# Kernel tuning notes

Measured on AMD Instinct MI355X. Metric: run time of the kernel, lower is better.

Reference implementation:

```python
import jax, jax.numpy as jnp
import numpy as np

B, NP, NM, C, H = 4, 256, 128, 128, 128
EPS = 1e-5

def layernorm(x, g, b):
    mu = jnp.mean(x, axis=-1, keepdims=True)
    var = jnp.var(x, axis=-1, keepdims=True)
    return (x - mu) * jax.lax.rsqrt(var + EPS) * g + b

def setup_inputs() -> dict:
    key = jax.random.key(0)
    ks = jax.random.split(key, 16)
    s = lambda d: 1.0 / np.sqrt(d)
    return {
        "z": jax.random.normal(ks[0], (B, NP, NM, C), jnp.float32),
        "z_mask": jnp.ones((B, NP, NM), jnp.float32),
        "pocket_pair": jax.random.normal(ks[1], (B, NP, NP, C), jnp.float32),
        "mol_pair": jax.random.normal(ks[2], (B, NM, NM, C), jnp.float32),
        "ln_g": jnp.ones((C,), jnp.float32), "ln_b": jnp.zeros((C,), jnp.float32),
        "lnh_g": jnp.ones((H,), jnp.float32), "lnh_b": jnp.zeros((H,), jnp.float32),
        "gw1": jax.random.uniform(ks[3], (C, H), jnp.float32, -s(C), s(C)),
        "gb1": jnp.zeros((H,), jnp.float32),
        "gw2": jax.random.uniform(ks[4], (C, H), jnp.float32, -s(C), s(C)),
        "gb2": jnp.zeros((H,), jnp.float32),
        "w1": jax.random.uniform(ks[5], (C, H), jnp.float32, -s(C), s(C)),
        "b1": jnp.zeros((H,), jnp.float32),
        "w2": jax.random.uniform(ks[6], (C, H), jnp.float32, -s(C), s(C)),
        "b2": jnp.zeros((H,), jnp.float32),
        "egw": jax.random.uniform(ks[7], (C, C), jnp.float32, -s(C), s(C)),
        "egb": jnp.zeros((C,), jnp.float32),
        "asw": jax.random.uniform(ks[8], (H, C), jnp.float32, -s(H), s(H)),
        "asb": jnp.zeros((C,), jnp.float32),
    }

def reference(z, z_mask, pocket_pair, mol_pair, ln_g, ln_b, lnh_g, lnh_b,
              gw1, gb1, gw2, gb2, w1, b1, w2, b2, egw, egb, asw, asb):
    m = z_mask[..., None]                      # [b,Np,Nm,1]
    zn = layernorm(z, ln_g, ln_b)              # [b,Np,Nm,C]
    pp = layernorm(pocket_pair, ln_g, ln_b)    # [b,Np,Np,C]
    mp = layernorm(mol_pair, ln_g, ln_b)       # [b,Nm,Nm,C]
    gate1 = lambda x: jax.nn.sigmoid(x @ gw1 + gb1) * (x @ w1 + b1)
    gate2 = lambda x: jax.nn.sigmoid(x @ gw2 + gb2) * (x @ w2 + b2)
    ab1 = gate1(zn) * m                        # [b,Np,Nm,H]
    ab2 = gate2(zn) * m                        # [b,Np,Nm,H]
    ppg = gate2(pp)                            # [b,Np,Np,H]
    mpg = gate1(mp)                            # [b,Nm,Nm,H]
    block1 = jnp.einsum('bikc,bkjc->bijc', ppg, ab1)   # [b,Np,Nm,H]
    block2 = jnp.einsum('bikc,bjkc->bijc', ab2, mpg)   # [b,Np,Nm,H]
    h = layernorm(block1 + block2, lnh_g, lnh_b)
    out = jax.nn.sigmoid(zn @ egw + egb) * (h @ asw + asb) * m
    return out
```

## Files before the change

kernel.cpp:

```cpp
#include <hip/hip_runtime.h>
#include <hip/hip_bf16.h>

#define DEVFN __device__ __forceinline__
using bf16 = __hip_bfloat16;
typedef __attribute__((ext_vector_type(8))) short short8;
typedef __attribute__((ext_vector_type(4))) float f32x4;
typedef __attribute__((ext_vector_type(4))) unsigned short us4;

constexpr int BB = 4, NP = 256, NM = 128, CC = 128, HH = 128;
constexpr float EPS = 1e-5f;

#define MFMA16(a,b,c) __builtin_amdgcn_mfma_f32_16x16x32_bf16((a),(b),(c),0,0,0)

DEVFN unsigned short bfbits(float v){ union{ bf16 b; unsigned short s; } u; u.b = __float2bfloat16(v); return u.s; }
DEVFN float bits2f(unsigned short s){ union{ unsigned int i; float f; } u; u.i = ((unsigned)s) << 16; return u.f; }
DEVFN float sigm(float x){ return 1.0f / (1.0f + __expf(-x)); }


__global__ __launch_bounds__(256)
void prep_weights_kernel(const float* __restrict__ gw1, const float* __restrict__ w1,
                         const float* __restrict__ gw2, const float* __restrict__ w2,
                         const float* __restrict__ egw, const float* __restrict__ asw,
                         bf16* __restrict__ wt)
{
  __shared__ float wl[128][129];
  const int bx = blockIdx.x;
  const float* W = (bx==0)?gw1 : (bx==1)?w1 : (bx==2)?gw2 : (bx==3)?w2 : (bx==4)?egw : asw;
  const int t = threadIdx.x;
  for (int i = 0; i < 16; ++i){
    int idx = t + 256*i;
    int k = idx >> 5, n0 = (idx & 31) * 4;
    float4 v = *reinterpret_cast<const float4*>(W + k*128 + n0);
    wl[k][n0] = v.x; wl[k][n0+1] = v.y; wl[k][n0+2] = v.z; wl[k][n0+3] = v.w;
  }
  __syncthreads();
  short* o = reinterpret_cast<short*>(wt) + bx * 16384;
  const int n = t >> 1, kh = t & 1;
  #pragma unroll
  for (int j = 0; j < 8; ++j){
    short8 p;
    #pragma unroll
    for (int u = 0; u < 8; ++u) p[u] = (short)bfbits(wl[kh*64 + j*8 + u][n]);
    *reinterpret_cast<short8*>(o + n*128 + kh*64 + j*8) = p;
  }
}

struct GateSmem {
  short xs[128*128];
  float lgb[2][128];
  float mk[128];
};

DEVFN void gate_pass(const char* xb, const float* mk, int t, long obase,
                     const short* wtg, const short* wtl,
                     const float* __restrict__ bgp, const float* __restrict__ blp,
                     bf16* outp)
{
  const int l = t & 63, w = t >> 6, lr = l & 15, lg = l >> 4;
  const int n0 = w * 32;
  short8 bgf[2][4], blf[2][4];
  #pragma unroll
  for (int nt = 0; nt < 2; ++nt)
    #pragma unroll
    for (int ks = 0; ks < 4; ++ks){
      int n = n0 + nt*16 + lr, ko = ks*32 + lg*8;
      bgf[nt][ks] = *reinterpret_cast<const short8*>(wtg + n*128 + ko);
      blf[nt][ks] = *reinterpret_cast<const short8*>(wtl + n*128 + ko);
    }
  float bgv[2] = { bgp[n0 + lr], bgp[n0 + 16 + lr] };
  float blv[2] = { blp[n0 + lr], blp[n0 + 16 + lr] };
  unsigned short* ob = reinterpret_cast<unsigned short*>(outp);

  for (int mt = 0; mt < 8; ++mt){
    f32x4 zv = {0.f,0.f,0.f,0.f};
    f32x4 ag0 = zv, ag1 = zv, al0 = zv, al1 = zv;
    #pragma unroll
    for (int ks = 0; ks < 4; ++ks){
      int m = mt*16 + lr, ko = ks*32 + lg*8;
      short8 a = *reinterpret_cast<const short8*>(xb + ((m*256 + ko*2) ^ ((m & 7) << 4)));
      ag0 = MFMA16(a, bgf[0][ks], ag0);
      al0 = MFMA16(a, blf[0][ks], al0);
      ag1 = MFMA16(a, bgf[1][ks], ag1);
      al1 = MFMA16(a, blf[1][ks], al1);
    }
    #pragma unroll
    for (int nt = 0; nt < 2; ++nt){
      f32x4 ag = nt ? ag1 : ag0, al = nt ? al1 : al0;
      int h = n0 + nt*16 + lr;
      us4 pk;
      #pragma unroll
      for (int rg = 0; rg < 4; ++rg){
        int rowl = mt*16 + lg*4 + rg;
        float val = sigm(ag[rg] + bgv[nt]) * (al[rg] + blv[nt]) * mk[rowl];
        pk[rg] = bfbits(val);
      }
      *reinterpret_cast<us4*>(ob + obase + h*128 + mt*16 + lg*4) = pk;
    }
  }
}

DEVFN void eg_pass(const char* xb, int t, long obase,
                   const short* wtg, const float* __restrict__ bgp, bf16* outp)
{
  const int l = t & 63, w = t >> 6, lr = l & 15, lg = l >> 4;
  const int n0 = w * 32;
  short8 bgf[2][4];
  #pragma unroll
  for (int nt = 0; nt < 2; ++nt)
    #pragma unroll
    for (int ks = 0; ks < 4; ++ks){
      int n = n0 + nt*16 + lr, ko = ks*32 + lg*8;
      bgf[nt][ks] = *reinterpret_cast<const short8*>(wtg + n*128 + ko);
    }
  float bgv[2] = { bgp[n0 + lr], bgp[n0 + 16 + lr] };
  unsigned short* ob = reinterpret_cast<unsigned short*>(outp);

  for (int mt = 0; mt < 8; ++mt){
    f32x4 zv = {0.f,0.f,0.f,0.f};
    f32x4 ag0 = zv, ag1 = zv;
    #pragma unroll
    for (int ks = 0; ks < 4; ++ks){
      int m = mt*16 + lr, ko = ks*32 + lg*8;
      short8 a = *reinterpret_cast<const short8*>(xb + ((m*256 + ko*2) ^ ((m & 7) << 4)));
      ag0 = MFMA16(a, bgf[0][ks], ag0);
      ag1 = MFMA16(a, bgf[1][ks], ag1);
    }
    #pragma unroll
    for (int nt = 0; nt < 2; ++nt){
      f32x4 ag = nt ? ag1 : ag0;
      int h = n0 + nt*16 + lr;
      us4 pk;
      #pragma unroll
      for (int rg = 0; rg < 4; ++rg) pk[rg] = bfbits(sigm(ag[rg] + bgv[nt]));
      *reinterpret_cast<us4*>(ob + obase + h*128 + mt*16 + lg*4) = pk;
    }
  }
}

constexpr int NZB = (BB*NP*NM)/128;
constexpr int NPB = (BB*NP*NP)/128;
constexpr int NMB = (BB*NM*NM)/128;

__global__ __launch_bounds__(256, 3)
void gate_all_kernel(const float* __restrict__ z, const float* __restrict__ zmask,
                     const float* __restrict__ pp, const float* __restrict__ mp,
                     const float* __restrict__ lng, const float* __restrict__ lnb,
                     const bf16* __restrict__ wt,
                     const float* __restrict__ gb1, const float* __restrict__ b1,
                     const float* __restrict__ gb2, const float* __restrict__ b2,
                     const float* __restrict__ egbv,
                     bf16* ab1, bf16* ab2, bf16* egp, bf16* ppg, bf16* mpg)
{
  __shared__ GateSmem sm;
  const int t = threadIdx.x;
  const short* wts = reinterpret_cast<const short*>(wt);

  int bx = blockIdx.x;
  const float* x; const float* mask = nullptr;
  long R; int npass = 1;
  const short *w1g, *w1l; const float *bg1v, *bl1v; bf16* o1;
  if (bx < NZB){
    x = z; mask = zmask; R = (long)NP*NM; npass = 3;
    w1g = wts + 0*16384; w1l = wts + 1*16384; bg1v = gb1; bl1v = b1; o1 = ab1;
  } else if (bx < NZB + NPB){
    bx -= NZB; x = pp; R = (long)NP*NP;
    w1g = wts + 2*16384; w1l = wts + 3*16384; bg1v = gb2; bl1v = b2; o1 = ppg;
  } else {
    bx -= NZB + NPB; x = mp; R = (long)NM*NM;
    w1g = wts + 0*16384; w1l = wts + 1*16384; bg1v = gb1; bl1v = b1; o1 = mpg;
  }
  const long row0 = (long)bx * 128;
  const int b = (int)(row0 / R);
  const long rowb = row0 - (long)b * R;
  const long obase = ((long)b * (R >> 7) + (rowb >> 7)) * 16384;

  if (t < 128){
    sm.lgb[0][t] = lng[t];
    sm.lgb[1][t] = lnb[t];
    sm.mk[t] = mask ? mask[row0 + t] : 1.0f;
  }

  const int r = t >> 1, hf = t & 1;
  const float4* xrow = reinterpret_cast<const float4*>(x + (row0 + r)*128 + hf*64);
  float4 vb[16];
  float s = 0.f, ss = 0.f;
  #pragma unroll
  for (int i = 0; i < 16; ++i){
    float4 v = xrow[i]; vb[i] = v;
    s  += v.x + v.y + v.z + v.w;
    ss += v.x*v.x + v.y*v.y + v.z*v.z + v.w*v.w;
  }
  s  += __shfl_xor(s, 1);
  ss += __shfl_xor(ss, 1);
  const float mu = s * (1.f/128.f);
  const float rsg = rsqrtf(ss * (1.f/128.f) - mu*mu + EPS);
  __syncthreads();
  {
    char* xbw = reinterpret_cast<char*>(sm.xs);
    #pragma unroll
    for (int j = 0; j < 8; ++j){
      float4 a = vb[2*j], c2 = vb[2*j+1];
      float vv[8] = {a.x, a.y, a.z, a.w, c2.x, c2.y, c2.z, c2.w};
      short8 p;
      #pragma unroll
      for (int u = 0; u < 8; ++u){
        int ch = hf*64 + j*8 + u;
        p[u] = (short)bfbits((vv[u] - mu) * rsg * sm.lgb[0][ch] + sm.lgb[1][ch]);
      }
      *reinterpret_cast<short8*>(xbw + ((r*256 + hf*128 + j*16) ^ ((r & 7) << 4))) = p;
    }
  }
  __syncthreads();

  const char* xb = reinterpret_cast<const char*>(sm.xs);
  gate_pass(xb, sm.mk, t, obase, w1g, w1l, bg1v, bl1v, o1);
  if (npass == 3){
    gate_pass(xb, sm.mk, t, obase, wts + 2*16384, wts + 3*16384, gb2, b2, ab2);
    eg_pass(xb, t, obase, wts + 4*16384, egbv, egp);
  }
}

DEVFN int b1swz(int j){ return (((j & 7) ^ ((j >> 3) & 7)) << 4); }

__global__ __launch_bounds__(256, 2)
void einsum_mfma_kernel(const bf16* __restrict__ ppg, const bf16* __restrict__ ab1,
                        const bf16* __restrict__ ab2, const bf16* __restrict__ mpg,
                        bf16* __restrict__ bsum)
{
  __shared__ short b1t[128*256];
  const int t = threadIdx.x, l = t & 63, w = t >> 6, lr = l & 15, lg = l >> 4;
  const int bc = blockIdx.x;
  const int b = bc >> 7, c = bc & 127;
  const short* A1s = reinterpret_cast<const short*>(ppg);
  const short* B1s = reinterpret_cast<const short*>(ab1);
  const short* A2s = reinterpret_cast<const short*>(ab2);
  const short* B2s = reinterpret_cast<const short*>(mpg);
  const long a1base = ((long)b*512*128 + c) * 128;
  const long b1base = ((long)b*256*128 + c) * 128;
  const long a2base = ((long)b*256*128 + c) * 128;
  const long b2base = ((long)b*128*128 + c) * 128;

  char* lb = reinterpret_cast<char*>(b1t);
  for (int it = 0; it < 16; ++it){
    int idx = t + 256*it;
    int k = idx >> 4, j0 = (idx & 15) * 8;
    short8 v = *reinterpret_cast<const short8*>(B1s + b1base + (long)k*16384 + j0);
    #pragma unroll
    for (int u = 0; u < 8; ++u){
      int j = j0 + u;
      *reinterpret_cast<short*>(lb + ((j*512 + k*2) ^ b1swz(j))) = v[u];
    }
  }
  __syncthreads();

  f32x4 zv = {0.f,0.f,0.f,0.f};
  f32x4 acc[4][8];
  #pragma unroll
  for (int i = 0; i < 4; ++i)
    #pragma unroll
    for (int j = 0; j < 8; ++j) acc[i][j] = zv;

  const int m0 = w * 64;
  for (int ks = 0; ks < 8; ++ks){
    int ko = ks*32 + lg*8;
    int koh = ko >> 7, kol = ko & 127;
    short8 af[4];
    #pragma unroll
    for (int mt = 0; mt < 4; ++mt){
      long m = m0 + mt*16 + lr;
      af[mt] = *reinterpret_cast<const short8*>(A1s + a1base + m*32768 + (long)koh*16384 + kol);
    }
    short8 bf[8];
    #pragma unroll
    for (int nt = 0; nt < 8; ++nt){
      int n = nt*16 + lr;
      bf[nt] = *reinterpret_cast<const short8*>(lb + ((n*512 + ko*2) ^ b1swz(n)));
    }
    #pragma unroll
    for (int mt = 0; mt < 4; ++mt)
      #pragma unroll
      for (int nt = 0; nt < 8; ++nt)
        acc[mt][nt] = MFMA16(af[mt], bf[nt], acc[mt][nt]);
  }
  for (int ks = 0; ks < 4; ++ks){
    int ko = ks*32 + lg*8;
    short8 af[4];
    #pragma unroll
    for (int mt = 0; mt < 4; ++mt){
      long m = m0 + mt*16 + lr;
      af[mt] = *reinterpret_cast<const short8*>(A2s + a2base + m*16384 + ko);
    }
    short8 bf[8];
    #pragma unroll
    for (int nt = 0; nt < 8; ++nt){
      long n = nt*16 + lr;
      bf[nt] = *reinterpret_cast<const short8*>(B2s + b2base + n*16384 + ko);
    }
    #pragma unroll
    for (int mt = 0; mt < 4; ++mt)
      #pragma unroll
      for (int nt = 0; nt < 8; ++nt)
        acc[mt][nt] = MFMA16(af[mt], bf[nt], acc[mt][nt]);
  }
  unsigned short* out = reinterpret_cast<unsigned short*>(bsum) + (long)bc * (NP*NM);
  #pragma unroll
  for (int mt = 0; mt < 4; ++mt)
    #pragma unroll
    for (int nt = 0; nt < 8; ++nt)
      #pragma unroll
      for (int rg = 0; rg < 4; ++rg)
        out[(m0 + mt*16 + lg*4 + rg)*128 + nt*16 + lr] = bfbits(acc[mt][nt][rg]);
}

__global__ __launch_bounds__(256, 2)
void final_mfma_kernel(const bf16* __restrict__ bsum, const bf16* __restrict__ eg,
                       const float* __restrict__ mask,
                       const float* __restrict__ lnhg, const float* __restrict__ lnhb,
                       const bf16* __restrict__ wt, const float* __restrict__ asb,
                       float* __restrict__ out)
{
  __shared__ struct {
    short xsT[128][72];
    short xs[64*128];
    float lgb[2][128];
    float ps[4][64], pss[4][64];
    float mu[64], rs[64], mk[64];
  } sm;
  const int t = threadIdx.x, l = t & 63, w = t >> 6, lr = l & 15, lg = l >> 4;
  const long row0 = (long)blockIdx.x * 64;
  const int b = (int)(row0 >> 15);
  const long rowb = row0 & 32767;

  if (t < 128){ sm.lgb[0][t] = lnhg[t]; sm.lgb[1][t] = lnhb[t]; }
  if (t < 64) sm.mk[t] = mask[row0 + t];

  const short* bs = reinterpret_cast<const short*>(bsum);
  #pragma unroll
  for (int i = 0; i < 4; ++i){
    int idx = t + 256*i;
    int c = idx >> 3, j8 = idx & 7;
    short8 v = *reinterpret_cast<const short8*>(bs + (long)(b*128 + c)*32768 + rowb + j8*8);
    *reinterpret_cast<short8*>(&sm.xsT[c][j8*8]) = v;
  }
  __syncthreads();
  {
    int ij = t & 63, q = t >> 6;
    float s = 0.f, ss = 0.f;
    #pragma unroll
    for (int k = 0; k < 32; ++k){
      float v = bits2f((unsigned short)sm.xsT[q*32 + k][ij]);
      s += v; ss += v*v;
    }
    sm.ps[q][ij] = s; sm.pss[q][ij] = ss;
  }
  __syncthreads();
  if (t < 64){
    float s  = sm.ps[0][t] + sm.ps[1][t] + sm.ps[2][t] + sm.ps[3][t];
    float ss = sm.pss[0][t] + sm.pss[1][t] + sm.pss[2][t] + sm.pss[3][t];
    float mu = s * (1.f/128.f);
    float var = ss * (1.f/128.f) - mu*mu;
    sm.mu[t] = mu; sm.rs[t] = rsqrtf(var + EPS);
  }
  __syncthreads();
  {
    int ij = t & 63, q = t >> 6;
    float mu = sm.mu[ij], rg2 = sm.rs[ij];
    char* xbw = reinterpret_cast<char*>(sm.xs);
    #pragma unroll
    for (int u = 0; u < 4; ++u){
      short8 p;
      #pragma unroll
      for (int e = 0; e < 8; ++e){
        int c = q*32 + u*8 + e;
        float v = bits2f((unsigned short)sm.xsT[c][ij]);
        p[e] = (short)bfbits((v - mu) * rg2 * sm.lgb[0][c] + sm.lgb[1][c]);
      }
      *reinterpret_cast<short8*>(xbw + ((ij*256 + q*64 + u*16) ^ ((ij & 7) << 4))) = p;
    }
  }
  __syncthreads();

  const short* aswt = reinterpret_cast<const short*>(wt) + 5*16384;
  f32x4 zv = {0.f,0.f,0.f,0.f};
  f32x4 acc[8];
  #pragma unroll
  for (int i = 0; i < 8; ++i) acc[i] = zv;
  const char* xb = reinterpret_cast<const char*>(sm.xs);
  #pragma unroll
  for (int ks = 0; ks < 4; ++ks){
    int m = w*16 + lr, ko = ks*32 + lg*8;
    short8 a = *reinterpret_cast<const short8*>(xb + ((m*256 + ko*2) ^ ((m & 7) << 4)));
    #pragma unroll
    for (int nt = 0; nt < 8; ++nt){
      short8 bfr = *reinterpret_cast<const short8*>(aswt + (nt*16 + lr)*128 + ko);
      acc[nt] = MFMA16(a, bfr, acc[nt]);
    }
  }
  const unsigned short* egb2 = reinterpret_cast<const unsigned short*>(eg);
  const long egbase = ((long)b*256 + (rowb >> 7)) * 16384;
  const int rsub = (int)(rowb & 64);
  #pragma unroll
  for (int nt = 0; nt < 8; ++nt){
    int co = nt*16 + lr;
    float bias = asb[co];
    us4 egv = *reinterpret_cast<const us4*>(egb2 + egbase + co*128 + rsub + w*16 + lg*4);
    #pragma unroll
    for (int rg = 0; rg < 4; ++rg){
      int rowl = w*16 + lg*4 + rg;
      float val = bits2f(egv[rg]) * (acc[nt][rg] + bias) * sm.mk[rowl];
      out[(row0 + rowl)*128 + co] = val;
    }
  }
}

extern "C" void kernel_launch(void* const* d_in, const int* in_sizes, int n_in,
                              void* d_out, int out_size, void* d_ws, size_t ws_size,
                              hipStream_t stream)
{
  const float* z     = (const float*)d_in[0];
  const float* zmask = (const float*)d_in[1];
  const float* pp    = (const float*)d_in[2];
  const float* mp    = (const float*)d_in[3];
  const float* ln_g  = (const float*)d_in[4];
  const float* ln_b  = (const float*)d_in[5];
  const float* lnh_g = (const float*)d_in[6];
  const float* lnh_b = (const float*)d_in[7];
  const float* gw1   = (const float*)d_in[8];
  const float* gb1   = (const float*)d_in[9];
  const float* gw2   = (const float*)d_in[10];
  const float* gb2   = (const float*)d_in[11];
  const float* w1    = (const float*)d_in[12];
  const float* b1    = (const float*)d_in[13];
  const float* w2    = (const float*)d_in[14];
  const float* b2    = (const float*)d_in[15];
  const float* egw   = (const float*)d_in[16];
  const float* egb   = (const float*)d_in[17];
  const float* asw   = (const float*)d_in[18];
  const float* asb   = (const float*)d_in[19];
  float* out = (float*)d_out;

  const size_t ZE = (size_t)BB*NP*NM*HH;
  const size_t PE = (size_t)BB*NP*NP*HH;
  const size_t ME = (size_t)BB*NM*NM*HH;
  char* ws = (char*)d_ws;
  size_t off = 0;
  bf16* wt   = (bf16*)(ws + off); off += 6 * 16384 * 2;
  bf16* ab1  = (bf16*)(ws + off); off += ZE * 2;
  bf16* ab2  = (bf16*)(ws + off); off += ZE * 2;
  bf16* egp  = (bf16*)(ws + off); off += ZE * 2;
  bf16* ppg  = (bf16*)(ws + off); off += PE * 2;
  bf16* mpg  = (bf16*)(ws + off); off += ME * 2;
  bf16* bsum = (bf16*)(ws + off); off += ZE * 2;
  if (ws_size < off) return;

  prep_weights_kernel<<<6, 256, 0, stream>>>(gw1, w1, gw2, w2, egw, asw, wt);

  gate_all_kernel<<<NZB + NPB + NMB, 256, 0, stream>>>(
      z, zmask, pp, mp, ln_g, ln_b, wt,
      gb1, b1, gb2, b2, egb,
      ab1, ab2, egp, ppg, mpg);

  einsum_mfma_kernel<<<BB*CC, 256, 0, stream>>>(ppg, ab1, ab2, mpg, bsum);

  final_mfma_kernel<<<(BB*NP*NM)/64, 256, 0, stream>>>(
      bsum, egp, zmask, lnh_g, lnh_b, wt, asb, out);
}
```

Measured before the change: 245.7 us.

## Process two row tiles per gate block, prefetching the second during compute

Each gate_all block now handles two consecutive 128-row tiles and the grid is halved. The second tile's fp32 input is loaded into registers before the first tile's gate and eg MFMA passes run, so global load latency overlaps with compute. The cost is that 64 extra floats per thread stay live across the MFMA passes. Under the launch bound of 3 blocks per SM this can raise register pressure or cause spills, and there are fewer blocks to balance load.

```diff
diff --git a/kernel.cpp b/kernel.cpp
--- a/kernel.cpp
+++ b/kernel.cpp
@@ -141,6 +141,23 @@
 constexpr int NPB = (BB*NP*NP)/128;
 constexpr int NMB = (BB*NM*NM)/128;
 
+DEVFN void ln_store(GateSmem& sm, const float4* vb, int r, int hf, float mu, float rsg)
+{
+  char* xbw = reinterpret_cast<char*>(sm.xs);
+  #pragma unroll
+  for (int j = 0; j < 8; ++j){
+    float4 a = vb[2*j], c2 = vb[2*j+1];
+    float vv[8] = {a.x, a.y, a.z, a.w, c2.x, c2.y, c2.z, c2.w};
+    short8 p;
+    #pragma unroll
+    for (int u = 0; u < 8; ++u){
+      int ch = hf*64 + j*8 + u;
+      p[u] = (short)bfbits((vv[u] - mu) * rsg * sm.lgb[0][ch] + sm.lgb[1][ch]);
+    }
+    *reinterpret_cast<short8*>(xbw + ((r*256 + hf*128 + j*16) ^ ((r & 7) << 4))) = p;
+  }
+}
+
 __global__ __launch_bounds__(256, 3)
 void gate_all_kernel(const float* __restrict__ z, const float* __restrict__ zmask,
                      const float* __restrict__ pp, const float* __restrict__ mp,
@@ -155,7 +172,7 @@
   const int t = threadIdx.x;
   const short* wts = reinterpret_cast<const short*>(wt);
 
-  int bx = blockIdx.x;
+  int bx = blockIdx.x * 2;
   const float* x; const float* mask = nullptr;
   long R; int npass = 1;
   const short *w1g, *w1l; const float *bg1v, *bl1v; bf16* o1;
@@ -170,9 +187,7 @@
     w1g = wts + 0*16384; w1l = wts + 1*16384; bg1v = gb1; bl1v = b1; o1 = mpg;
   }
   const long row0 = (long)bx * 128;
-  const int b = (int)(row0 / R);
-  const long rowb = row0 - (long)b * R;
-  const long obase = ((long)b * (R >> 7) + (rowb >> 7)) * 16384;
+  const int r = t >> 1, hf = t & 1;
 
   if (t < 128){
     sm.lgb[0][t] = lng[t];
@@ -180,43 +195,79 @@
     sm.mk[t] = mask ? mask[row0 + t] : 1.0f;
   }
 
-  const int r = t >> 1, hf = t & 1;
-  const float4* xrow = reinterpret_cast<const float4*>(x + (row0 + r)*128 + hf*64);
   float4 vb[16];
-  float s = 0.f, ss = 0.f;
-  #pragma unroll
-  for (int i = 0; i < 16; ++i){
-    float4 v = xrow[i]; vb[i] = v;
-    s  += v.x + v.y + v.z + v.w;
-    ss += v.x*v.x + v.y*v.y + v.z*v.z + v.w*v.w;
-  }
-  s  += __shfl_xor(s, 1);
-  ss += __shfl_xor(ss, 1);
-  const float mu = s * (1.f/128.f);
-  const float rsg = rsqrtf(ss * (1.f/128.f) - mu*mu + EPS);
-  __syncthreads();
-  {
-    char* xbw = reinterpret_cast<char*>(sm.xs);
-    #pragma unroll
-    for (int j = 0; j < 8; ++j){
-      float4 a = vb[2*j], c2 = vb[2*j+1];
-      float vv[8] = {a.x, a.y, a.z, a.w, c2.x, c2.y, c2.z, c2.w};
-      short8 p;
-      #pragma unroll
-      for (int u = 0; u < 8; ++u){
-        int ch = hf*64 + j*8 + u;
-        p[u] = (short)bfbits((vv[u] - mu) * rsg * sm.lgb[0][ch] + sm.lgb[1][ch]);
-      }
-      *reinterpret_cast<short8*>(xbw + ((r*256 + hf*128 + j*16) ^ ((r & 7) << 4))) = p;
-    }
-  }
-  __syncthreads();
-
-  const char* xb = reinterpret_cast<const char*>(sm.xs);
-  gate_pass(xb, sm.mk, t, obase, w1g, w1l, bg1v, bl1v, o1);
-  if (npass == 3){
-    gate_pass(xb, sm.mk, t, obase, wts + 2*16384, wts + 3*16384, gb2, b2, ab2);
-    eg_pass(xb, t, obase, wts + 4*16384, egbv, egp);
+  {
+    const float4* xr = reinterpret_cast<const float4*>(x + (row0 + r)*128 + hf*64);
+    #pragma unroll
+    for (int i = 0; i < 16; ++i) vb[i] = xr[i];
+  }
+
+  {
+    float s = 0.f, ss = 0.f;
+    #pragma unroll
+    for (int i = 0; i < 16; ++i){
+      float4 v = vb[i];
+      s  += v.x + v.y + v.z + v.w;
+      ss += v.x*v.x + v.y*v.y + v.z*v.z + v.w*v.w;
+    }
+    s  += __shfl_xor(s, 1);
+    ss += __shfl_xor(ss, 1);
+    const float mu = s * (1.f/128.f);
+    const float rsg = rsqrtf(ss * (1.f/128.f) - mu*mu + EPS);
+    __syncthreads();
+    ln_store(sm, vb, r, hf, mu, rsg);
+  }
+  __syncthreads();
+
+  {
+    const float4* xr = reinterpret_cast<const float4*>(x + (row0 + 128 + r)*128 + hf*64);
+    #pragma unroll
+    for (int i = 0; i < 16; ++i) vb[i] = xr[i];
+  }
+
+  {
+    const int b = (int)(row0 / R);
+    const long rowb = row0 - (long)b * R;
+    const long obase = ((long)b * (R >> 7) + (rowb >> 7)) * 16384;
+    const char* xb = reinterpret_cast<const char*>(sm.xs);
+    gate_pass(xb, sm.mk, t, obase, w1g, w1l, bg1v, bl1v, o1);
+    if (npass == 3){
+      gate_pass(xb, sm.mk, t, obase, wts + 2*16384, wts + 3*16384, gb2, b2, ab2);
+      eg_pass(xb, t, obase, wts + 4*16384, egbv, egp);
+    }
+  }
+
+  __builtin_amdgcn_sched_barrier(0);
+
+  const long row1 = row0 + 128;
+  {
+    float s = 0.f, ss = 0.f;
+    #pragma unroll
+    for (int i = 0; i < 16; ++i){
+      float4 v = vb[i];
+      s  += v.x + v.y + v.z + v.w;
+      ss += v.x*v.x + v.y*v.y + v.z*v.z + v.w*v.w;
+    }
+    s  += __shfl_xor(s, 1);
+    ss += __shfl_xor(ss, 1);
+    const float mu = s * (1.f/128.f);
+    const float rsg = rsqrtf(ss * (1.f/128.f) - mu*mu + EPS);
+    __syncthreads();
+    if (mask && t < 128) sm.mk[t] = mask[row1 + t];
+    ln_store(sm, vb, r, hf, mu, rsg);
+  }
+  __syncthreads();
+
+  {
+    const int b = (int)(row1 / R);
+    const long rowb = row1 - (long)b * R;
+    const long obase = ((long)b * (R >> 7) + (rowb >> 7)) * 16384;
+    const char* xb = reinterpret_cast<const char*>(sm.xs);
+    gate_pass(xb, sm.mk, t, obase, w1g, w1l, bg1v, bl1v, o1);
+    if (npass == 3){
+      gate_pass(xb, sm.mk, t, obase, wts + 2*16384, wts + 3*16384, gb2, b2, ab2);
+      eg_pass(xb, t, obase, wts + 4*16384, egbv, egp);
+    }
   }
 }
 
@@ -455,7 +506,7 @@
 
   prep_weights_kernel<<<6, 256, 0, stream>>>(gw1, w1, gw2, w2, egw, asw, wt);
 
-  gate_all_kernel<<<NZB + NPB + NMB, 256, 0, stream>>>(
+  gate_all_kernel<<<(NZB + NPB + NMB)/2, 256, 0, stream>>>(
       z, zmask, pp, mp, ln_g, ln_b, wt,
       gb1, b1, gb2, b2, egb,
       ab1, ab2, egp, ppg, mpg);
```

After: 278.3 us. +13.3%, slower.
